# Kernel optimization log

Measured on AMD Instinct MI355X. Metric: run time of the kernel, lower is better.

Reference implementation:

```python
import jax, jax.numpy as jnp
import numpy as np

B, T, TR, D, H = 8, 1024, 256, 1024, 16
HS = D // H  # head size = 64
FF = 4 * D


def _ln(x, g, b, eps=1e-5):
    m = jnp.mean(x, axis=-1, keepdims=True)
    v = jnp.mean((x - m) ** 2, axis=-1, keepdims=True)
    return (x - m) * jax.lax.rsqrt(v + eps) * g + b


def setup_inputs() -> dict:
    key = jax.random.key(0)
    ks = jax.random.split(key, 24)
    w = lambda i, shape: jax.random.normal(ks[i], shape, dtype=jnp.float32) * 0.02
    return {
        "x": jax.random.normal(ks[0], (B, T, D), dtype=jnp.float32),
        # reduced positional embedding table (gathered by arange == table itself)
        "pos_emb": w(1, (TR, D)),
        # inner standard Block params
        "blk_ln1_g": jnp.ones((D,), jnp.float32), "blk_ln1_b": jnp.zeros((D,), jnp.float32),
        "blk_wq": w(2, (H, D, HS)), "blk_wk": w(3, (H, D, HS)), "blk_wv": w(4, (H, D, HS)),
        "blk_wo": w(5, (D, D)), "blk_bo": jnp.zeros((D,), jnp.float32),
        "blk_ln2_g": jnp.ones((D,), jnp.float32), "blk_ln2_b": jnp.zeros((D,), jnp.float32),
        "blk_w1": w(6, (D, FF)), "blk_b1": jnp.zeros((FF,), jnp.float32),
        "blk_w2": w(7, (FF, D)), "blk_b2": jnp.zeros((D,), jnp.float32),
        # compressing cross-attention params
        "ln1_g": jnp.ones((D,), jnp.float32), "ln1_b": jnp.zeros((D,), jnp.float32),
        "ca_wq": w(8, (H, D, HS)), "ca_wk": w(9, (H, D, HS)), "ca_wv": w(10, (H, D, HS)),
        "ca_wo": w(11, (D, D)), "ca_bo": jnp.zeros((D,), jnp.float32),
        "ln2_g": jnp.ones((D,), jnp.float32), "ln2_b": jnp.zeros((D,), jnp.float32),
        "ff_w1": w(12, (D, FF)), "ff_b1": jnp.zeros((FF,), jnp.float32),
        "ff_w2": w(13, (FF, D)), "ff_b2": jnp.zeros((D,), jnp.float32),
    }


def reference(x, pos_emb, blk_ln1_g, blk_ln1_b, blk_wq, blk_wk, blk_wv, blk_wo, blk_bo,
              blk_ln2_g, blk_ln2_b, blk_w1, blk_b1, blk_w2, blk_b2,
              ln1_g, ln1_b, ca_wq, ca_wk, ca_wv, ca_wo, ca_bo,
              ln2_g, ln2_b, ff_w1, ff_b1, ff_w2, ff_b2):
    b, t, c = x.shape
    scale = c ** -0.5  # matches q @ k^T * c**-0.5 in source

    # ---- inner standard Block: y = x + sa(ln1(x)); y = y + ffwd(ln2(y)) ----
    h = _ln(x, blk_ln1_g, blk_ln1_b)
    q = jnp.einsum('btc,hcs->bhts', h, blk_wq)
    k = jnp.einsum('btc,hcs->bhts', h, blk_wk)
    v = jnp.einsum('btc,hcs->bhts', h, blk_wv)
    wei = jnp.einsum('bhts,bhus->bhtu', q, k) * scale
    causal = jnp.tril(jnp.ones((t, t), dtype=bool))
    wei = jax.nn.softmax(jnp.where(causal, wei, -jnp.inf), axis=-1)
    att = jnp.einsum('bhtu,bhus->bhts', wei, v)
    att = att.transpose(0, 2, 1, 3).reshape(b, t, c) @ blk_wo + blk_bo
    y = x + att
    h2 = _ln(y, blk_ln2_g, blk_ln2_b)
    y = y + (jax.nn.relu(h2 @ blk_w1 + blk_b1) @ blk_w2 + blk_b2)

    # outer residual in CompressingBlock.forward
    x = x + y

    # ---- compressing cross-attention: queries/values from x, keys from pos emb ----
    h1 = _ln(x, ln1_g, ln1_b)
    q = jnp.einsum('btc,hcs->bhts', h1, ca_wq)
    kk = jnp.einsum('rc,hcs->hrs', pos_emb, ca_wk)  # same for every batch
    v = jnp.einsum('btc,hcs->bhts', h1, ca_wv)
    wei = jnp.einsum('bhts,hrs->bhtr', q, kk) * scale  # [b,h,t,tr]
    tr = pos_emb.shape[0]
    mask = jnp.tril(jnp.ones((t, tr), dtype=bool))  # tril[:t,:tr]
    wei = jax.nn.softmax(jnp.where(mask, wei, -jnp.inf), axis=-1)
    # transpose then wei^T @ v -> compressed sequence length tr
    out = jnp.einsum('bhtr,bhts->bhrs', wei, v)
    out = out.transpose(0, 2, 1, 3).reshape(b, tr, c) @ ca_wo + ca_bo

    # ---- final FFN with residual ----
    h3 = _ln(out, ln2_g, ln2_b)
    out = out + (jax.nn.relu(h3 @ ff_w1 + ff_b1) @ ff_w2 + ff_b2)
    return out
```

## Files before the change

### kernel.cpp

```cpp
#include <hip/hip_runtime.h>
#include <stdint.h>

typedef unsigned short u16;
typedef __attribute__((ext_vector_type(8))) short short8;
typedef __attribute__((ext_vector_type(4))) float f32x4;

#define MFMA16(A,B,C) __builtin_amdgcn_mfma_f32_16x16x32_bf16(A,B,C,0,0,0)

static __device__ __forceinline__ u16 f2bf(float f) {
  union { float f; unsigned u; } v; v.f = f;
  unsigned r = v.u + 0x7FFFu + ((v.u >> 16) & 1u);
  return (u16)(r >> 16);
}

static __device__ __forceinline__ void gload16(const void* g, void* l) {
  __builtin_amdgcn_global_load_lds(
      (const __attribute__((address_space(1))) void*)(uintptr_t)g,
      (__attribute__((address_space(3))) void*)(uint32_t)(uintptr_t)l,
      16, 0, 0);
}

static __device__ __forceinline__ int xcd_swz() {
  const int gx = gridDim.x, gy = gridDim.y, nwg = gx * gy;
  const int orig = blockIdx.y * gx + blockIdx.x;
  const int q = nwg >> 3, rm = nwg & 7, xcd = orig & 7, idx = orig >> 3;
  return (xcd < rm ? xcd * (q + 1) : rm * (q + 1) + (xcd - rm) * q) + idx;
}

#define PHASEP(BUFO, KH, STAGE_STMT, TAIL_STMT) do { \
  short8 af_[4], bf_[4]; \
  _Pragma("unroll") \
  for (int mf = 0; mf < 4; ++mf) { \
    const int r = wm0 + mf * 16 + colL; \
    af_[mf] = *(const short8*)&lds[(BUFO) + ((KH) << 12) + r * 32 + ((kgr ^ ((r >> 1) & 3)) << 3)]; \
  } \
  _Pragma("unroll") \
  for (int nf = 0; nf < 4; ++nf) { \
    const int r = wn0 + nf * 16 + colL; \
    bf_[nf] = *(const short8*)&lds[(BUFO) + 8192 + ((KH) << 12) + r * 32 + ((kgr ^ ((r >> 1) & 3)) << 3)]; \
  } \
  STAGE_STMT; \
  __builtin_amdgcn_s_barrier(); \
  asm volatile("s_waitcnt lgkmcnt(0)" ::: "memory"); \
  __builtin_amdgcn_sched_barrier(0); \
  __builtin_amdgcn_s_setprio(1); \
  _Pragma("unroll") \
  for (int mf = 0; mf < 4; ++mf) \
    _Pragma("unroll") \
    for (int nf = 0; nf < 4; ++nf) \
      acc[mf][nf] = MFMA16(af_[mf], bf_[nf], acc[mf][nf]); \
  __builtin_amdgcn_s_setprio(0); \
  __builtin_amdgcn_sched_barrier(0); \
  TAIL_STMT; \
  __builtin_amdgcn_s_barrier(); \
} while (0)

__global__ __launch_bounds__(256) void gemm128p(
    const u16* __restrict__ A, const u16* __restrict__ Wt,
    float* __restrict__ Cf, u16* __restrict__ Cb,
    const float* __restrict__ bias,
    const float* __restrict__ res1, const float* __restrict__ res2,
    int M, int N, int K, int relu)
{
  __shared__ u16 lds[32768];
  const int tid = threadIdx.x;
  const int wid = tid >> 6, lane = tid & 63;
  const int colL = lane & 15, kgr = lane >> 4;
  const int wm0 = (wid & 1) * 64, wn0 = (wid >> 1) * 64;
  const int w = xcd_swz();
  const int m0 = (w / gridDim.y) * 128, n0 = (w % gridDim.y) * 128;
  const int NT = K >> 6;
  f32x4 acc[4][4] = {};

  auto stageP = [&](int t_, int kh) {
    const int kb = t_ * 64 + kh * 32;
    const int baseA = ((t_ & 1) << 14) + (kh << 12);
#pragma unroll
    for (int i = 0; i < 2; ++i) {
      const int c = i * 256 + tid;
      const int row = c >> 2, slot = c & 3;
      const int cs = kb + ((slot ^ ((row >> 1) & 3)) << 3);
      gload16(A  + (size_t)(m0 + row) * K + cs,
              &lds[baseA + ((i * 256 + wid * 64) << 3)]);
      gload16(Wt + (size_t)(n0 + row) * K + cs,
              &lds[baseA + 8192 + ((i * 256 + wid * 64) << 3)]);
    }
  };

  stageP(0, 0); stageP(0, 1); stageP(1, 0);
  asm volatile("s_waitcnt vmcnt(8)" ::: "memory");
  __builtin_amdgcn_s_barrier();

  for (int t = 0; t < NT; ++t) {
    const int bufo = (t & 1) << 14;
    PHASEP(bufo, 0,
           if (t + 1 < NT) stageP(t + 1, 1),
           if (t + 1 < NT) { asm volatile("s_waitcnt vmcnt(8)" ::: "memory"); }
           else            { asm volatile("s_waitcnt vmcnt(0)" ::: "memory"); } );
    PHASEP(bufo, 1,
           if (t + 2 < NT) stageP(t + 2, 0),
           if (t < NT - 2)       { asm volatile("s_waitcnt vmcnt(8)" ::: "memory"); }
           else if (t == NT - 2) { asm volatile("s_waitcnt vmcnt(4)" ::: "memory"); }
           else                  { asm volatile("s_waitcnt vmcnt(0)" ::: "memory"); } );
  }

#pragma unroll
  for (int mf = 0; mf < 4; ++mf) {
#pragma unroll
    for (int nf = 0; nf < 4; ++nf) {
      const int n = n0 + wn0 + nf * 16 + colL;
      const float bv = bias ? bias[n] : 0.f;
#pragma unroll
      for (int rr = 0; rr < 4; ++rr) {
        const int m = m0 + wm0 + mf * 16 + kgr * 4 + rr;
        const size_t off = (size_t)m * N + n;
        float v = acc[mf][nf][rr] + bv;
        if (res1) v += res1[off];
        if (res2) v += res2[off];
        if (relu) v = fmaxf(v, 0.f);
        if (Cf) Cf[off] = v; else Cb[off] = f2bf(v);
      }
    }
  }
}

__global__ __launch_bounds__(256) void ln_rows(
    const float* __restrict__ x, const float* __restrict__ g,
    const float* __restrict__ bt, u16* __restrict__ out)
{
  const int row = blockIdx.x, tid = threadIdx.x;
  const float4 v = ((const float4*)(x + (size_t)row * 1024))[tid];
  float s  = v.x + v.y + v.z + v.w;
  float ss = v.x * v.x + v.y * v.y + v.z * v.z + v.w * v.w;
#pragma unroll
  for (int off = 32; off; off >>= 1) {
    s  += __shfl_xor(s, off);
    ss += __shfl_xor(ss, off);
  }
  __shared__ float red[8];
  const int wid = tid >> 6, lane = tid & 63;
  if (lane == 0) { red[wid] = s; red[4 + wid] = ss; }
  __syncthreads();
  s  = red[0] + red[1] + red[2] + red[3];
  ss = red[4] + red[5] + red[6] + red[7];
  const float mean = s * 0.0009765625f;
  const float var  = ss * 0.0009765625f - mean * mean;
  const float rstd = rsqrtf(var + 1e-5f);
  const float4 gg = ((const float4*)g)[tid];
  const float4 bb = ((const float4*)bt)[tid];
  uint2 ov;
  ov.x = (unsigned)f2bf((v.x - mean) * rstd * gg.x + bb.x) |
         ((unsigned)f2bf((v.y - mean) * rstd * gg.y + bb.y) << 16);
  ov.y = (unsigned)f2bf((v.z - mean) * rstd * gg.z + bb.z) |
         ((unsigned)f2bf((v.w - mean) * rstd * gg.w + bb.w) << 16);
  *(uint2*)(out + (size_t)row * 1024 + tid * 4) = ov;
}

__global__ __launch_bounds__(256) void transpose_w(
    const float* __restrict__ in, u16* __restrict__ out, int R, int C)
{
  __shared__ float t[32][33];
  const int c0 = blockIdx.x * 32, r0 = blockIdx.y * 32;
  const int tx = threadIdx.x & 31, ty = threadIdx.x >> 5;
#pragma unroll
  for (int i = 0; i < 32; i += 8)
    t[ty + i][tx] = in[(size_t)(r0 + ty + i) * C + c0 + tx];
  __syncthreads();
#pragma unroll
  for (int i = 0; i < 32; i += 8)
    out[(size_t)(c0 + ty + i) * R + r0 + tx] = f2bf(t[tx][ty + i]);
}

__global__ __launch_bounds__(256) void pack_head_w(
    const float* __restrict__ w, u16* __restrict__ out)
{
  __shared__ float t[32][33];
  const int h = blockIdx.z;
  const int s0 = blockIdx.x * 32, c0 = blockIdx.y * 32;
  const int tx = threadIdx.x & 31, ty = threadIdx.x >> 5;
#pragma unroll
  for (int i = 0; i < 32; i += 8)
    t[ty + i][tx] = w[((size_t)h * 1024 + c0 + ty + i) * 64 + s0 + tx];
  __syncthreads();
#pragma unroll
  for (int i = 0; i < 32; i += 8)
    out[((size_t)h * 64 + s0 + ty + i) * 1024 + c0 + tx] = f2bf(t[tx][ty + i]);
}

__global__ __launch_bounds__(256) void cvt_bf16(
    const float* __restrict__ in, u16* __restrict__ out)
{
  const int i = blockIdx.x * blockDim.x + threadIdx.x;
  const float4 v = ((const float4*)in)[i];
  uint2 ov;
  ov.x = (unsigned)f2bf(v.x) | ((unsigned)f2bf(v.y) << 16);
  ov.y = (unsigned)f2bf(v.z) | ((unsigned)f2bf(v.w) << 16);
  *(uint2*)(out + (size_t)i * 4) = ov;
}

__global__ __launch_bounds__(256) void vtrans(
    const u16* __restrict__ src, u16* __restrict__ dst, int coloff, int ld)
{
  __shared__ u16 tile[64][65];
  const int t0 = blockIdx.x * 64, h = blockIdx.y, b = blockIdx.z;
  const int lr = threadIdx.x >> 4;
  const int lc = (threadIdx.x & 15) * 4;
#pragma unroll
  for (int i = 0; i < 64; i += 16) {
    const u16* sp = src + (size_t)(b * 1024 + t0 + lr + i) * ld + coloff + h * 64 + lc;
    const uint2 v = *(const uint2*)sp;
    tile[lr + i][lc + 0] = (u16)(v.x & 0xffff);
    tile[lr + i][lc + 1] = (u16)(v.x >> 16);
    tile[lr + i][lc + 2] = (u16)(v.y & 0xffff);
    tile[lr + i][lc + 3] = (u16)(v.y >> 16);
  }
  __syncthreads();
#pragma unroll
  for (int i = 0; i < 64; i += 16) {
    const int s = lr + i;
    uint2 ov;
    ov.x = (unsigned)tile[lc + 0][s] | ((unsigned)tile[lc + 1][s] << 16);
    ov.y = (unsigned)tile[lc + 2][s] | ((unsigned)tile[lc + 3][s] << 16);
    *(uint2*)(dst + (size_t)((b * 16 + h) * 64 + s) * 1024 + t0 + lc) = ov;
  }
}

__global__ __launch_bounds__(512) void attn_inner(
    const u16* __restrict__ qkv, const u16* __restrict__ vt,
    u16* __restrict__ att)
{
  __shared__ u16 Kl[128 * 64];
  __shared__ u16 Vl[64 * 128];
  __shared__ u16 Pl[8 * 16 * 128];
  const int p = blockIdx.x, h = blockIdx.y, b = blockIdx.z;
  const int tid = threadIdx.x, wid = tid >> 6, lane = tid & 63;
  const int col = lane & 15, kgr = lane >> 4;
  const float scale = 0.03125f;
  u16* pw = &Pl[wid * 2048];

  auto run_q = [&](int tb) {
    short8 qf[2];
    {
      const int trow = tb * 128 + wid * 16 + col;
      const u16* qp = qkv + (size_t)(b * 1024 + trow) * 3072 + h * 64 + kgr * 8;
      qf[0] = *(const short8*)qp;
      qf[1] = *(const short8*)(qp + 32);
    }
    f32x4 o[4] = {};
    float mrun[4], lrun[4];
#pragma unroll
    for (int r = 0; r < 4; ++r) { mrun[r] = -1e30f; lrun[r] = 0.f; }

    for (int kt = 0; kt <= tb * 128; kt += 128) {
#pragma unroll
      for (int i = 0; i < 2; ++i) {
        const int e = i * 4096 + tid * 8;
        const int rk = e >> 6, uk = (e >> 3) & 7;
        gload16(qkv + (size_t)(b * 1024 + kt + rk) * 3072 + 1024 + h * 64 +
                    ((uk ^ (rk & 7)) << 3),
                &Kl[i * 4096 + wid * 512]);
        const int rv = e >> 7, uv = (e >> 3) & 15;
        gload16(vt + (size_t)((b * 16 + h) * 64 + rv) * 1024 + kt +
                    ((uv ^ (rv & 7)) << 3),
                &Vl[i * 4096 + wid * 512]);
      }
      __syncthreads();
      f32x4 s[8];
#pragma unroll
      for (int nt = 0; nt < 8; ++nt) {
        const int rk = nt * 16 + col;
        const short8 k0 = *(const short8*)&Kl[rk * 64 + ((kgr ^ (rk & 7)) << 3)];
        const short8 k1 = *(const short8*)&Kl[rk * 64 + (((kgr + 4) ^ (rk & 7)) << 3)];
        f32x4 a = {};
        a = MFMA16(qf[0], k0, a);
        a = MFMA16(qf[1], k1, a);
        s[nt] = a;
      }
      float mx[4];
#pragma unroll
      for (int r = 0; r < 4; ++r) mx[r] = -1e30f;
      const int tbase = tb * 128 + wid * 16 + kgr * 4;
      if (kt == tb * 128) {
#pragma unroll
        for (int nt = 0; nt < 8; ++nt) {
          const int kp = kt + nt * 16 + col;
#pragma unroll
          for (int r = 0; r < 4; ++r) {
            float v = s[nt][r] * scale;
            if (kp > tbase + r) v = -1e30f;
            s[nt][r] = v;
            mx[r] = fmaxf(mx[r], v);
          }
        }
      } else {
#pragma unroll
        for (int nt = 0; nt < 8; ++nt)
#pragma unroll
          for (int r = 0; r < 4; ++r) {
            const float v = s[nt][r] * scale;
            s[nt][r] = v;
            mx[r] = fmaxf(mx[r], v);
          }
      }
#pragma unroll
      for (int r = 0; r < 4; ++r)
#pragma unroll
        for (int off = 1; off < 16; off <<= 1)
          mx[r] = fmaxf(mx[r], __shfl_xor(mx[r], off));
      float f[4], rs[4];
#pragma unroll
      for (int r = 0; r < 4; ++r) {
        const float mn = fmaxf(mrun[r], mx[r]);
        f[r] = __expf(mrun[r] - mn);
        mrun[r] = mn;
        rs[r] = 0.f;
      }
#pragma unroll
      for (int nt = 0; nt < 8; ++nt)
#pragma unroll
        for (int r = 0; r < 4; ++r) {
          const float pv = __expf(s[nt][r] - mrun[r]);
          s[nt][r] = pv;
          rs[r] += pv;
        }
#pragma unroll
      for (int r = 0; r < 4; ++r) {
#pragma unroll
        for (int off = 1; off < 16; off <<= 1)
          rs[r] += __shfl_xor(rs[r], off);
        lrun[r] = lrun[r] * f[r] + rs[r];
      }
#pragma unroll
      for (int st = 0; st < 4; ++st)
#pragma unroll
        for (int r = 0; r < 4; ++r)
          o[st][r] *= f[r];
#pragma unroll
      for (int nt = 0; nt < 8; ++nt)
#pragma unroll
        for (int r = 0; r < 4; ++r) {
          const int rp = kgr * 4 + r;
          pw[rp * 128 + ((nt * 16 + col) ^ ((rp & 7) << 3))] = f2bf(s[nt][r]);
        }
#pragma unroll
      for (int ks = 0; ks < 4; ++ks) {
        const short8 pa = *(const short8*)&pw[col * 128 +
            ((ks * 32 + kgr * 8) ^ ((col & 7) << 3))];
#pragma unroll
        for (int st = 0; st < 4; ++st) {
          const int rv = st * 16 + col;
          const short8 vb = *(const short8*)&Vl[rv * 128 +
              (((ks * 4 + kgr) ^ (rv & 7)) << 3)];
          o[st] = MFMA16(pa, vb, o[st]);
        }
      }
      __syncthreads();
    }
#pragma unroll
    for (int r = 0; r < 4; ++r) {
      const float inv = 1.f / lrun[r];
      const int t = tb * 128 + wid * 16 + kgr * 4 + r;
#pragma unroll
      for (int st = 0; st < 4; ++st)
        att[(size_t)(b * 1024 + t) * 1024 + h * 64 + st * 16 + col] =
            f2bf(o[st][r] * inv);
    }
  };

  run_q(7 - p);
  run_q(p);
}

__global__ __launch_bounds__(512) void attn_cross(
    const u16* __restrict__ qv, const u16* __restrict__ kk,
    const u16* __restrict__ vt, u16* __restrict__ outc)
{
  __shared__ u16 KKl[256 * 64];
  __shared__ u16 Vl[64 * 128];
  __shared__ u16 PTl[256 * 128];
  const int h = blockIdx.x, b = blockIdx.y;
  const int tid = threadIdx.x, wid = tid >> 6, lane = tid & 63;
  const int col = lane & 15, kgr = lane >> 4;
  const float scale = 0.03125f;
#pragma unroll
  for (int i = 0; i < 4; ++i) {
    const int e = i * 4096 + tid * 8;
    const int rk = e >> 6, uk = (e >> 3) & 7;
    gload16(kk + (size_t)rk * 1024 + h * 64 + ((uk ^ (rk & 7)) << 3),
            &KKl[i * 4096 + wid * 512]);
  }
  f32x4 oacc[2][4] = {};
  for (int tt = 0; tt < 8; ++tt) {
    const int t0 = tt * 128;
#pragma unroll
    for (int i = 0; i < 2; ++i) {
      const int e = i * 4096 + tid * 8;
      const int rv = e >> 7, uv = (e >> 3) & 15;
      gload16(vt + (size_t)((b * 16 + h) * 64 + rv) * 1024 + t0 +
                  ((uv ^ (rv & 7)) << 3),
              &Vl[i * 4096 + wid * 512]);
    }
    short8 qf0, qf1;
    {
      const int trow = t0 + wid * 16 + col;
      const u16* qp = qv + (size_t)(b * 1024 + trow) * 2048 + h * 64 + kgr * 8;
      qf0 = *(const short8*)qp;
      qf1 = *(const short8*)(qp + 32);
    }
    __syncthreads();
    f32x4 s[16];
#pragma unroll
    for (int rt = 0; rt < 16; ++rt) {
      const int rk = rt * 16 + col;
      const short8 k0 = *(const short8*)&KKl[rk * 64 + ((kgr ^ (rk & 7)) << 3)];
      const short8 k1 = *(const short8*)&KKl[rk * 64 + (((kgr + 4) ^ (rk & 7)) << 3)];
      f32x4 a = {};
      a = MFMA16(qf0, k0, a);
      a = MFMA16(qf1, k1, a);
      s[rt] = a;
    }
    float mx[4];
#pragma unroll
    for (int r = 0; r < 4; ++r) mx[r] = -1e30f;
    const int tbase = t0 + wid * 16 + kgr * 4;
    if (t0 < 256) {
#pragma unroll
      for (int rt = 0; rt < 16; ++rt) {
        const int rp = rt * 16 + col;
#pragma unroll
        for (int r = 0; r < 4; ++r) {
          float v = s[rt][r] * scale;
          if (rp > tbase + r) v = -1e30f;
          s[rt][r] = v;
          mx[r] = fmaxf(mx[r], v);
        }
      }
    } else {
#pragma unroll
      for (int rt = 0; rt < 16; ++rt)
#pragma unroll
        for (int r = 0; r < 4; ++r) {
          const float v = s[rt][r] * scale;
          s[rt][r] = v;
          mx[r] = fmaxf(mx[r], v);
        }
    }
#pragma unroll
    for (int r = 0; r < 4; ++r)
#pragma unroll
      for (int off = 1; off < 16; off <<= 1)
        mx[r] = fmaxf(mx[r], __shfl_xor(mx[r], off));
    float sm[4];
#pragma unroll
    for (int r = 0; r < 4; ++r) sm[r] = 0.f;
#pragma unroll
    for (int rt = 0; rt < 16; ++rt)
#pragma unroll
      for (int r = 0; r < 4; ++r) {
        const float pv = __expf(s[rt][r] - mx[r]);
        s[rt][r] = pv;
        sm[r] += pv;
      }
#pragma unroll
    for (int r = 0; r < 4; ++r) {
#pragma unroll
      for (int off = 1; off < 16; off <<= 1)
        sm[r] += __shfl_xor(sm[r], off);
      sm[r] = 1.f / sm[r];
    }
#pragma unroll
    for (int rt = 0; rt < 16; ++rt)
#pragma unroll
      for (int r = 0; r < 4; ++r) {
        const int rpt = rt * 16 + col;
        PTl[rpt * 128 + ((wid * 16 + kgr * 4 + r) ^ ((rpt & 7) << 3))] =
            f2bf(s[rt][r] * sm[r]);
      }
    __syncthreads();
#pragma unroll
    for (int rr = 0; rr < 2; ++rr) {
      const int rb = (wid * 2 + rr) * 16;
#pragma unroll
      for (int ks = 0; ks < 4; ++ks) {
        const int rpt = rb + col;
        const short8 pa = *(const short8*)&PTl[rpt * 128 +
            ((ks * 32 + kgr * 8) ^ ((rpt & 7) << 3))];
#pragma unroll
        for (int st = 0; st < 4; ++st) {
          const int rv = st * 16 + col;
          const short8 vb = *(const short8*)&Vl[rv * 128 +
              (((ks * 4 + kgr) ^ (rv & 7)) << 3)];
          oacc[rr][st] = MFMA16(pa, vb, oacc[rr][st]);
        }
      }
    }
    __syncthreads();
  }
#pragma unroll
  for (int rr = 0; rr < 2; ++rr)
#pragma unroll
    for (int st = 0; st < 4; ++st)
#pragma unroll
      for (int r = 0; r < 4; ++r) {
        const int rpos = (wid * 2 + rr) * 16 + kgr * 4 + r;
        outc[(size_t)(b * 256 + rpos) * 1024 + h * 64 + st * 16 + col] =
            f2bf(oacc[rr][st][r]);
      }
}

extern "C" void kernel_launch(void* const* d_in, const int* in_sizes, int n_in,
                              void* d_out, int out_size, void* d_ws, size_t ws_size,
                              hipStream_t stream)
{
  const float* x     = (const float*)d_in[0];
  const float* pos   = (const float*)d_in[1];
  const float* bln1g = (const float*)d_in[2];
  const float* bln1b = (const float*)d_in[3];
  const float* bwq   = (const float*)d_in[4];
  const float* bwk   = (const float*)d_in[5];
  const float* bwv   = (const float*)d_in[6];
  const float* bwo   = (const float*)d_in[7];
  const float* bbo   = (const float*)d_in[8];
  const float* bln2g = (const float*)d_in[9];
  const float* bln2b = (const float*)d_in[10];
  const float* bw1   = (const float*)d_in[11];
  const float* bb1   = (const float*)d_in[12];
  const float* bw2   = (const float*)d_in[13];
  const float* bb2   = (const float*)d_in[14];
  const float* ln1g  = (const float*)d_in[15];
  const float* ln1b  = (const float*)d_in[16];
  const float* cwq   = (const float*)d_in[17];
  const float* cwk   = (const float*)d_in[18];
  const float* cwv   = (const float*)d_in[19];
  const float* cwo   = (const float*)d_in[20];
  const float* cbo   = (const float*)d_in[21];
  const float* cln2g = (const float*)d_in[22];
  const float* cln2b = (const float*)d_in[23];
  const float* fw1   = (const float*)d_in[24];
  const float* fb1   = (const float*)d_in[25];
  const float* fw2   = (const float*)d_in[26];
  const float* fb2   = (const float*)d_in[27];

  char* ws = (char*)d_ws;
  size_t off = 0;
  auto alloc = [&](size_t bytes) -> void* {
    void* p = ws + off; off += (bytes + 255) & ~(size_t)255; return p;
  };
  u16* wqkv_t = (u16*)alloc((size_t)3072 * 1024 * 2);
  u16* wo_t   = (u16*)alloc((size_t)1024 * 1024 * 2);
  u16* w1_t   = (u16*)alloc((size_t)4096 * 1024 * 2);
  u16* w2_t   = (u16*)alloc((size_t)1024 * 4096 * 2);
  u16* cwqv_t = (u16*)alloc((size_t)2048 * 1024 * 2);
  u16* cwk_t  = (u16*)alloc((size_t)1024 * 1024 * 2);
  u16* cwo_t  = (u16*)alloc((size_t)1024 * 1024 * 2);
  u16* fw1_t  = (u16*)alloc((size_t)4096 * 1024 * 2);
  u16* fw2_t  = (u16*)alloc((size_t)1024 * 4096 * 2);
  u16* pos_bf = (u16*)alloc((size_t)256 * 1024 * 2);
  u16* kkb    = (u16*)alloc((size_t)256 * 1024 * 2);
  u16* act_ln = (u16*)alloc((size_t)8192 * 1024 * 2);
  u16* qkv    = (u16*)alloc((size_t)8192 * 3072 * 2);
  u16* att    = (u16*)alloc((size_t)8192 * 1024 * 2);
  u16* ffb    = (u16*)alloc((size_t)8192 * 4096 * 2);
  float* yb   = (float*)alloc((size_t)8192 * 1024 * 4);
  if (ws_size < off) return;
  float* x2   = (float*)qkv;
  u16*   qv   = qkv;
  u16*   vt   = ffb;
  u16*   outc = att;
  float* zb   = yb;
  float* outp = (float*)d_out;

  const dim3 B256(256), B512(512);
  pack_head_w<<<dim3(2, 32, 16), B256, 0, stream>>>(bwq, wqkv_t);
  pack_head_w<<<dim3(2, 32, 16), B256, 0, stream>>>(bwk, wqkv_t + 1024 * 1024);
  pack_head_w<<<dim3(2, 32, 16), B256, 0, stream>>>(bwv, wqkv_t + 2048 * 1024);
  transpose_w<<<dim3(32, 32),  B256, 0, stream>>>(bwo, wo_t, 1024, 1024);
  transpose_w<<<dim3(128, 32), B256, 0, stream>>>(bw1, w1_t, 1024, 4096);
  transpose_w<<<dim3(32, 128), B256, 0, stream>>>(bw2, w2_t, 4096, 1024);
  pack_head_w<<<dim3(2, 32, 16), B256, 0, stream>>>(cwq, cwqv_t);
  pack_head_w<<<dim3(2, 32, 16), B256, 0, stream>>>(cwv, cwqv_t + 1024 * 1024);
  pack_head_w<<<dim3(2, 32, 16), B256, 0, stream>>>(cwk, cwk_t);
  transpose_w<<<dim3(32, 32),  B256, 0, stream>>>(cwo, cwo_t, 1024, 1024);
  transpose_w<<<dim3(128, 32), B256, 0, stream>>>(fw1, fw1_t, 1024, 4096);
  transpose_w<<<dim3(32, 128), B256, 0, stream>>>(fw2, fw2_t, 4096, 1024);
  cvt_bf16<<<dim3(256), B256, 0, stream>>>(pos, pos_bf);

  ln_rows<<<dim3(8192), B256, 0, stream>>>(x, bln1g, bln1b, act_ln);
  gemm128p<<<dim3(64, 24), B256, 0, stream>>>(act_ln, wqkv_t, nullptr, qkv,
      nullptr, nullptr, nullptr, 8192, 3072, 1024, 0);
  vtrans<<<dim3(16, 16, 8), B256, 0, stream>>>(qkv, vt, 2048, 3072);
  attn_inner<<<dim3(4, 16, 8), B512, 0, stream>>>(qkv, vt, att);
  gemm128p<<<dim3(64, 8), B256, 0, stream>>>(att, wo_t, yb, nullptr,
      bbo, x, nullptr, 8192, 1024, 1024, 0);
  ln_rows<<<dim3(8192), B256, 0, stream>>>(yb, bln2g, bln2b, act_ln);
  gemm128p<<<dim3(64, 32), B256, 0, stream>>>(act_ln, w1_t, nullptr, ffb,
      bb1, nullptr, nullptr, 8192, 4096, 1024, 1);
  gemm128p<<<dim3(64, 8), B256, 0, stream>>>(ffb, w2_t, x2, nullptr,
      bb2, yb, x, 8192, 1024, 4096, 0);

  ln_rows<<<dim3(8192), B256, 0, stream>>>(x2, ln1g, ln1b, act_ln);
  gemm128p<<<dim3(64, 16), B256, 0, stream>>>(act_ln, cwqv_t, nullptr, qv,
      nullptr, nullptr, nullptr, 8192, 2048, 1024, 0);
  gemm128p<<<dim3(2, 8), B256, 0, stream>>>(pos_bf, cwk_t, nullptr, kkb,
      nullptr, nullptr, nullptr, 256, 1024, 1024, 0);
  vtrans<<<dim3(16, 16, 8), B256, 0, stream>>>(qv, vt, 1024, 2048);
  attn_cross<<<dim3(16, 8), B512, 0, stream>>>(qv, kkb, vt, outc);
  gemm128p<<<dim3(16, 8), B256, 0, stream>>>(outc, cwo_t, zb, nullptr,
      cbo, nullptr, nullptr, 2048, 1024, 1024, 0);

  ln_rows<<<dim3(2048), B256, 0, stream>>>(zb, cln2g, cln2b, act_ln);
  gemm128p<<<dim3(16, 32), B256, 0, stream>>>(act_ln, fw1_t, nullptr, ffb,
      fb1, nullptr, nullptr, 2048, 4096, 1024, 1);
  gemm128p<<<dim3(16, 8), B256, 0, stream>>>(ffb, fw2_t, outp, nullptr,
      fb2, zb, nullptr, 2048, 1024, 4096, 0);
}
```

Measured before the change: 720.3 us.

## Load GEMM A operand directly from global into registers, stage only B in LDS

The bf16 GEMM kernel stops staging the A tile through LDS. Each wave now reads its A fragments directly from global memory into registers, double-buffered across the K half-steps, while only the weight (B) tile still goes through LDS via global_load_lds. This halves LDS use and raises the launch-bounds occupancy hint to 3 blocks per CU, aiming to cut LDS traffic and overlap more work. In exchange, A reads from global are less coalesced and are duplicated across waves that share rows, and their latency sits directly in front of the MFMAs. The vmcnt wait counts were retuned to match the new load mix.

```diff
diff --git a/kernel.cpp b/kernel.cpp
--- a/kernel.cpp
+++ b/kernel.cpp
@@ -27,19 +27,14 @@
   return (xcd < rm ? xcd * (q + 1) : rm * (q + 1) + (xcd - rm) * q) + idx;
 }
 
-#define PHASEP(BUFO, KH, STAGE_STMT, TAIL_STMT) do { \
-  short8 af_[4], bf_[4]; \
-  _Pragma("unroll") \
-  for (int mf = 0; mf < 4; ++mf) { \
-    const int r = wm0 + mf * 16 + colL; \
-    af_[mf] = *(const short8*)&lds[(BUFO) + ((KH) << 12) + r * 32 + ((kgr ^ ((r >> 1) & 3)) << 3)]; \
-  } \
+#define GPHASE(BUFO, KH, AF, PRE_STMT, TAIL_STMT) do { \
+  short8 bf_[4]; \
   _Pragma("unroll") \
   for (int nf = 0; nf < 4; ++nf) { \
     const int r = wn0 + nf * 16 + colL; \
-    bf_[nf] = *(const short8*)&lds[(BUFO) + 8192 + ((KH) << 12) + r * 32 + ((kgr ^ ((r >> 1) & 3)) << 3)]; \
+    bf_[nf] = *(const short8*)&lds[(BUFO) + ((KH) << 12) + r * 32 + ((kgr ^ ((r >> 1) & 3)) << 3)]; \
   } \
-  STAGE_STMT; \
+  PRE_STMT; \
   __builtin_amdgcn_s_barrier(); \
   asm volatile("s_waitcnt lgkmcnt(0)" ::: "memory"); \
   __builtin_amdgcn_sched_barrier(0); \
@@ -48,21 +43,21 @@
   for (int mf = 0; mf < 4; ++mf) \
     _Pragma("unroll") \
     for (int nf = 0; nf < 4; ++nf) \
-      acc[mf][nf] = MFMA16(af_[mf], bf_[nf], acc[mf][nf]); \
+      acc[mf][nf] = MFMA16(AF[mf], bf_[nf], acc[mf][nf]); \
   __builtin_amdgcn_s_setprio(0); \
   __builtin_amdgcn_sched_barrier(0); \
   TAIL_STMT; \
   __builtin_amdgcn_s_barrier(); \
 } while (0)
 
-__global__ __launch_bounds__(256) void gemm128p(
+__global__ __launch_bounds__(256, 3) void gemm128p(
     const u16* __restrict__ A, const u16* __restrict__ Wt,
     float* __restrict__ Cf, u16* __restrict__ Cb,
     const float* __restrict__ bias,
     const float* __restrict__ res1, const float* __restrict__ res2,
     int M, int N, int K, int relu)
 {
-  __shared__ u16 lds[32768];
+  __shared__ u16 lds[16384];
   const int tid = threadIdx.x;
   const int wid = tid >> 6, lane = tid & 63;
   const int colL = lane & 15, kgr = lane >> 4;
@@ -72,36 +67,49 @@
   const int NT = K >> 6;
   f32x4 acc[4][4] = {};
 
-  auto stageP = [&](int t_, int kh) {
+  const u16* ap0 = A + (size_t)(m0 + wm0 +  0 + colL) * K + kgr * 8;
+  const u16* ap1 = A + (size_t)(m0 + wm0 + 16 + colL) * K + kgr * 8;
+  const u16* ap2 = A + (size_t)(m0 + wm0 + 32 + colL) * K + kgr * 8;
+  const u16* ap3 = A + (size_t)(m0 + wm0 + 48 + colL) * K + kgr * 8;
+
+  auto stageB = [&](int t_, int kh) {
     const int kb = t_ * 64 + kh * 32;
-    const int baseA = ((t_ & 1) << 14) + (kh << 12);
+    const int base = ((t_ & 1) << 13) + (kh << 12);
 #pragma unroll
     for (int i = 0; i < 2; ++i) {
       const int c = i * 256 + tid;
       const int row = c >> 2, slot = c & 3;
-      const int cs = kb + ((slot ^ ((row >> 1) & 3)) << 3);
-      gload16(A  + (size_t)(m0 + row) * K + cs,
-              &lds[baseA + ((i * 256 + wid * 64) << 3)]);
-      gload16(Wt + (size_t)(n0 + row) * K + cs,
-              &lds[baseA + 8192 + ((i * 256 + wid * 64) << 3)]);
+      gload16(Wt + (size_t)(n0 + row) * K + kb + ((slot ^ ((row >> 1) & 3)) << 3),
+              &lds[base + ((i * 256 + wid * 64) << 3)]);
     }
   };
 
-  stageP(0, 0); stageP(0, 1); stageP(1, 0);
-  asm volatile("s_waitcnt vmcnt(8)" ::: "memory");
+  short8 afA[4], afB[4];
+  auto loadA = [&](short8* dst, int t_, int kh) {
+    const int ko = t_ * 64 + kh * 32;
+    dst[0] = *(const short8*)(ap0 + ko);
+    dst[1] = *(const short8*)(ap1 + ko);
+    dst[2] = *(const short8*)(ap2 + ko);
+    dst[3] = *(const short8*)(ap3 + ko);
+  };
+
+  stageB(0, 0); stageB(0, 1); stageB(1, 0);
+  asm volatile("s_waitcnt vmcnt(4)" ::: "memory");
+  loadA(afA, 0, 0);
   __builtin_amdgcn_s_barrier();
 
   for (int t = 0; t < NT; ++t) {
-    const int bufo = (t & 1) << 14;
-    PHASEP(bufo, 0,
-           if (t + 1 < NT) stageP(t + 1, 1),
-           if (t + 1 < NT) { asm volatile("s_waitcnt vmcnt(8)" ::: "memory"); }
-           else            { asm volatile("s_waitcnt vmcnt(0)" ::: "memory"); } );
-    PHASEP(bufo, 1,
-           if (t + 2 < NT) stageP(t + 2, 0),
-           if (t < NT - 2)       { asm volatile("s_waitcnt vmcnt(8)" ::: "memory"); }
-           else if (t == NT - 2) { asm volatile("s_waitcnt vmcnt(4)" ::: "memory"); }
-           else                  { asm volatile("s_waitcnt vmcnt(0)" ::: "memory"); } );
+    const int bufo = (t & 1) << 13;
+    GPHASE(bufo, 0, afA,
+           { if (t + 1 < NT) stageB(t + 1, 1); loadA(afB, t, 1); },
+           { if (t + 1 < NT) { asm volatile("s_waitcnt vmcnt(12)" ::: "memory"); }
+             else            { asm volatile("s_waitcnt vmcnt(8)"  ::: "memory"); } });
+    GPHASE(bufo, 1, afB,
+           { if (t + 2 < NT) stageB(t + 2, 0);
+             if (t + 1 < NT) loadA(afA, t + 1, 0); },
+           { if (t + 2 < NT)      { asm volatile("s_waitcnt vmcnt(12)" ::: "memory"); }
+             else if (t + 1 < NT) { asm volatile("s_waitcnt vmcnt(10)" ::: "memory"); }
+             else                 { asm volatile("s_waitcnt vmcnt(0)"  ::: "memory"); } });
   }
 
 #pragma unroll
```

Result: slower. 1.028 ms (+42.7%).

## Switch GEMMs to 256x128 tiles with triple-buffered K=32 LDS pipeline

Applied to the files above, without the earlier changes.

Replaces the 128x128 double-buffered GEMM with a 256x128 tile where each wave computes 128x64 (8x4 MFMA fragments). The K loop now stages 32-wide slices into three rotating LDS buffers with a two-deep prefetch. Launch bounds ask for two blocks per CU. The larger M tile raises arithmetic intensity and halves the number of blocks. In exchange it doubles accumulator registers and produces fewer workgroups for the small 2048-row and 256-row GEMMs.

```diff
diff --git a/kernel.cpp b/kernel.cpp
--- a/kernel.cpp
+++ b/kernel.cpp
@@ -27,17 +27,17 @@
   return (xcd < rm ? xcd * (q + 1) : rm * (q + 1) + (xcd - rm) * q) + idx;
 }
 
-#define PHASEP(BUFO, KH, STAGE_STMT, TAIL_STMT) do { \
-  short8 af_[4], bf_[4]; \
+#define GPH(CUR, STAGE_STMT, TAIL_STMT) do { \
+  short8 af_[8], bf_[4]; \
   _Pragma("unroll") \
-  for (int mf = 0; mf < 4; ++mf) { \
+  for (int mf = 0; mf < 8; ++mf) { \
     const int r = wm0 + mf * 16 + colL; \
-    af_[mf] = *(const short8*)&lds[(BUFO) + ((KH) << 12) + r * 32 + ((kgr ^ ((r >> 1) & 3)) << 3)]; \
+    af_[mf] = *(const short8*)&lds[(CUR) + r * 32 + ((kgr ^ ((r >> 1) & 3)) << 3)]; \
   } \
   _Pragma("unroll") \
   for (int nf = 0; nf < 4; ++nf) { \
     const int r = wn0 + nf * 16 + colL; \
-    bf_[nf] = *(const short8*)&lds[(BUFO) + 8192 + ((KH) << 12) + r * 32 + ((kgr ^ ((r >> 1) & 3)) << 3)]; \
+    bf_[nf] = *(const short8*)&lds[(CUR) + (256 + r) * 32 + ((kgr ^ ((r >> 1) & 3)) << 3)]; \
   } \
   STAGE_STMT; \
   __builtin_amdgcn_s_barrier(); \
@@ -45,7 +45,7 @@
   __builtin_amdgcn_sched_barrier(0); \
   __builtin_amdgcn_s_setprio(1); \
   _Pragma("unroll") \
-  for (int mf = 0; mf < 4; ++mf) \
+  for (int mf = 0; mf < 8; ++mf) \
     _Pragma("unroll") \
     for (int nf = 0; nf < 4; ++nf) \
       acc[mf][nf] = MFMA16(af_[mf], bf_[nf], acc[mf][nf]); \
@@ -55,57 +55,56 @@
   __builtin_amdgcn_s_barrier(); \
 } while (0)
 
-__global__ __launch_bounds__(256) void gemm128p(
+__global__ __launch_bounds__(256, 2) void gemm256n(
     const u16* __restrict__ A, const u16* __restrict__ Wt,
     float* __restrict__ Cf, u16* __restrict__ Cb,
     const float* __restrict__ bias,
     const float* __restrict__ res1, const float* __restrict__ res2,
     int M, int N, int K, int relu)
 {
-  __shared__ u16 lds[32768];
+  __shared__ u16 lds[36864];
   const int tid = threadIdx.x;
   const int wid = tid >> 6, lane = tid & 63;
   const int colL = lane & 15, kgr = lane >> 4;
-  const int wm0 = (wid & 1) * 64, wn0 = (wid >> 1) * 64;
+  const int wm0 = (wid & 1) * 128, wn0 = (wid >> 1) * 64;
   const int w = xcd_swz();
-  const int m0 = (w / gridDim.y) * 128, n0 = (w % gridDim.y) * 128;
-  const int NT = K >> 6;
-  f32x4 acc[4][4] = {};
-
-  auto stageP = [&](int t_, int kh) {
-    const int kb = t_ * 64 + kh * 32;
-    const int baseA = ((t_ & 1) << 14) + (kh << 12);
-#pragma unroll
-    for (int i = 0; i < 2; ++i) {
+  const int m0 = (w / gridDim.y) * 256, n0 = (w % gridDim.y) * 128;
+  const int NT = K >> 5;
+  f32x4 acc[8][4] = {};
+
+  auto stage = [&](int t_, int bufo) {
+    const int kb = t_ * 32;
+#pragma unroll
+    for (int i = 0; i < 4; ++i) {
       const int c = i * 256 + tid;
       const int row = c >> 2, slot = c & 3;
-      const int cs = kb + ((slot ^ ((row >> 1) & 3)) << 3);
-      gload16(A  + (size_t)(m0 + row) * K + cs,
-              &lds[baseA + ((i * 256 + wid * 64) << 3)]);
-      gload16(Wt + (size_t)(n0 + row) * K + cs,
-              &lds[baseA + 8192 + ((i * 256 + wid * 64) << 3)]);
+      gload16(A + (size_t)(m0 + row) * K + kb + ((slot ^ ((row >> 1) & 3)) << 3),
+              &lds[bufo + ((i * 256 + wid * 64) << 3)]);
+    }
+#pragma unroll
+    for (int i = 4; i < 6; ++i) {
+      const int c = i * 256 + tid;
+      const int row = c >> 2, slot = c & 3;
+      gload16(Wt + (size_t)(n0 + row - 256) * K + kb + ((slot ^ ((row >> 1) & 3)) << 3),
+              &lds[bufo + ((i * 256 + wid * 64) << 3)]);
     }
   };
 
-  stageP(0, 0); stageP(0, 1); stageP(1, 0);
-  asm volatile("s_waitcnt vmcnt(8)" ::: "memory");
+  int c0 = 0, c1 = 12288, c2 = 24576;
+  stage(0, c0); stage(1, c1);
+  asm volatile("s_waitcnt vmcnt(6)" ::: "memory");
   __builtin_amdgcn_s_barrier();
 
   for (int t = 0; t < NT; ++t) {
-    const int bufo = (t & 1) << 14;
-    PHASEP(bufo, 0,
-           if (t + 1 < NT) stageP(t + 1, 1),
-           if (t + 1 < NT) { asm volatile("s_waitcnt vmcnt(8)" ::: "memory"); }
-           else            { asm volatile("s_waitcnt vmcnt(0)" ::: "memory"); } );
-    PHASEP(bufo, 1,
-           if (t + 2 < NT) stageP(t + 2, 0),
-           if (t < NT - 2)       { asm volatile("s_waitcnt vmcnt(8)" ::: "memory"); }
-           else if (t == NT - 2) { asm volatile("s_waitcnt vmcnt(4)" ::: "memory"); }
-           else                  { asm volatile("s_waitcnt vmcnt(0)" ::: "memory"); } );
+    GPH(c0,
+        { if (t + 2 < NT) stage(t + 2, c2); },
+        { if (t + 2 < NT) { asm volatile("s_waitcnt vmcnt(6)" ::: "memory"); }
+          else            { asm volatile("s_waitcnt vmcnt(0)" ::: "memory"); } });
+    const int tmp = c0; c0 = c1; c1 = c2; c2 = tmp;
   }
 
 #pragma unroll
-  for (int mf = 0; mf < 4; ++mf) {
+  for (int mf = 0; mf < 8; ++mf) {
 #pragma unroll
     for (int nf = 0; nf < 4; ++nf) {
       const int n = n0 + wn0 + nf * 16 + colL;
@@ -586,31 +585,31 @@
   cvt_bf16<<<dim3(256), B256, 0, stream>>>(pos, pos_bf);
 
   ln_rows<<<dim3(8192), B256, 0, stream>>>(x, bln1g, bln1b, act_ln);
-  gemm128p<<<dim3(64, 24), B256, 0, stream>>>(act_ln, wqkv_t, nullptr, qkv,
+  gemm256n<<<dim3(32, 24), B256, 0, stream>>>(act_ln, wqkv_t, nullptr, qkv,
       nullptr, nullptr, nullptr, 8192, 3072, 1024, 0);
   vtrans<<<dim3(16, 16, 8), B256, 0, stream>>>(qkv, vt, 2048, 3072);
   attn_inner<<<dim3(4, 16, 8), B512, 0, stream>>>(qkv, vt, att);
-  gemm128p<<<dim3(64, 8), B256, 0, stream>>>(att, wo_t, yb, nullptr,
+  gemm256n<<<dim3(32, 8), B256, 0, stream>>>(att, wo_t, yb, nullptr,
       bbo, x, nullptr, 8192, 1024, 1024, 0);
   ln_rows<<<dim3(8192), B256, 0, stream>>>(yb, bln2g, bln2b, act_ln);
-  gemm128p<<<dim3(64, 32), B256, 0, stream>>>(act_ln, w1_t, nullptr, ffb,
+  gemm256n<<<dim3(32, 32), B256, 0, stream>>>(act_ln, w1_t, nullptr, ffb,
       bb1, nullptr, nullptr, 8192, 4096, 1024, 1);
-  gemm128p<<<dim3(64, 8), B256, 0, stream>>>(ffb, w2_t, x2, nullptr,
+  gemm256n<<<dim3(32, 8), B256, 0, stream>>>(ffb, w2_t, x2, nullptr,
       bb2, yb, x, 8192, 1024, 4096, 0);
 
   ln_rows<<<dim3(8192), B256, 0, stream>>>(x2, ln1g, ln1b, act_ln);
-  gemm128p<<<dim3(64, 16), B256, 0, stream>>>(act_ln, cwqv_t, nullptr, qv,
+  gemm256n<<<dim3(32, 16), B256, 0, stream>>>(act_ln, cwqv_t, nullptr, qv,
       nullptr, nullptr, nullptr, 8192, 2048, 1024, 0);
-  gemm128p<<<dim3(2, 8), B256, 0, stream>>>(pos_bf, cwk_t, nullptr, kkb,
+  gemm256n<<<dim3(1, 8), B256, 0, stream>>>(pos_bf, cwk_t, nullptr, kkb,
       nullptr, nullptr, nullptr, 256, 1024, 1024, 0);
   vtrans<<<dim3(16, 16, 8), B256, 0, stream>>>(qv, vt, 1024, 2048);
   attn_cross<<<dim3(16, 8), B512, 0, stream>>>(qv, kkb, vt, outc);
-  gemm128p<<<dim3(16, 8), B256, 0, stream>>>(outc, cwo_t, zb, nullptr,
+  gemm256n<<<dim3(8, 8), B256, 0, stream>>>(outc, cwo_t, zb, nullptr,
       cbo, nullptr, nullptr, 2048, 1024, 1024, 0);
 
   ln_rows<<<dim3(2048), B256, 0, stream>>>(zb, cln2g, cln2b, act_ln);
-  gemm128p<<<dim3(16, 32), B256, 0, stream>>>(act_ln, fw1_t, nullptr, ffb,
+  gemm256n<<<dim3(8, 32), B256, 0, stream>>>(act_ln, fw1_t, nullptr, ffb,
       fb1, nullptr, nullptr, 2048, 4096, 1024, 1);
-  gemm128p<<<dim3(16, 8), B256, 0, stream>>>(ffb, fw2_t, outp, nullptr,
+  gemm256n<<<dim3(8, 8), B256, 0, stream>>>(ffb, fw2_t, outp, nullptr,
       fb2, zb, nullptr, 2048, 1024, 4096, 0);
 }
```

After: 800.6 us. 11.2% more time.

## Restructure GEMM K-loop into triple-buffered rotating LDS stages of 32

Applied to the files above, without the earlier changes.

Replaces the double-buffered 64-wide K tile (split into two 32-wide halves) with a three-slot ring of 32-wide K stages that rotate each iteration, prefetching two stages ahead. LDS use drops from 64KB to 48KB per block, which may allow higher occupancy and simplifies the wait-count logic. In exchange the in-flight prefetch depth is slightly lower (one stage of loads outstanding vs. two halves) and the loop runs twice as many iterations.

```diff
diff --git a/kernel.cpp b/kernel.cpp
--- a/kernel.cpp
+++ b/kernel.cpp
@@ -27,17 +27,17 @@
   return (xcd < rm ? xcd * (q + 1) : rm * (q + 1) + (xcd - rm) * q) + idx;
 }
 
-#define PHASEP(BUFO, KH, STAGE_STMT, TAIL_STMT) do { \
+#define GPH(CUR, STAGE_STMT, TAIL_STMT) do { \
   short8 af_[4], bf_[4]; \
   _Pragma("unroll") \
   for (int mf = 0; mf < 4; ++mf) { \
     const int r = wm0 + mf * 16 + colL; \
-    af_[mf] = *(const short8*)&lds[(BUFO) + ((KH) << 12) + r * 32 + ((kgr ^ ((r >> 1) & 3)) << 3)]; \
+    af_[mf] = *(const short8*)&lds[(CUR) + r * 32 + ((kgr ^ ((r >> 1) & 3)) << 3)]; \
   } \
   _Pragma("unroll") \
   for (int nf = 0; nf < 4; ++nf) { \
     const int r = wn0 + nf * 16 + colL; \
-    bf_[nf] = *(const short8*)&lds[(BUFO) + 8192 + ((KH) << 12) + r * 32 + ((kgr ^ ((r >> 1) & 3)) << 3)]; \
+    bf_[nf] = *(const short8*)&lds[(CUR) + 4096 + r * 32 + ((kgr ^ ((r >> 1) & 3)) << 3)]; \
   } \
   STAGE_STMT; \
   __builtin_amdgcn_s_barrier(); \
@@ -62,46 +62,41 @@
     const float* __restrict__ res1, const float* __restrict__ res2,
     int M, int N, int K, int relu)
 {
-  __shared__ u16 lds[32768];
+  __shared__ u16 lds[24576];
   const int tid = threadIdx.x;
   const int wid = tid >> 6, lane = tid & 63;
   const int colL = lane & 15, kgr = lane >> 4;
   const int wm0 = (wid & 1) * 64, wn0 = (wid >> 1) * 64;
   const int w = xcd_swz();
   const int m0 = (w / gridDim.y) * 128, n0 = (w % gridDim.y) * 128;
-  const int NT = K >> 6;
+  const int U = K >> 5;
   f32x4 acc[4][4] = {};
 
-  auto stageP = [&](int t_, int kh) {
-    const int kb = t_ * 64 + kh * 32;
-    const int baseA = ((t_ & 1) << 14) + (kh << 12);
+  auto stageP = [&](int u, int bufo) {
+    const int kb = u * 32;
 #pragma unroll
     for (int i = 0; i < 2; ++i) {
       const int c = i * 256 + tid;
       const int row = c >> 2, slot = c & 3;
       const int cs = kb + ((slot ^ ((row >> 1) & 3)) << 3);
       gload16(A  + (size_t)(m0 + row) * K + cs,
-              &lds[baseA + ((i * 256 + wid * 64) << 3)]);
+              &lds[bufo + ((i * 256 + wid * 64) << 3)]);
       gload16(Wt + (size_t)(n0 + row) * K + cs,
-              &lds[baseA + 8192 + ((i * 256 + wid * 64) << 3)]);
+              &lds[bufo + 4096 + ((i * 256 + wid * 64) << 3)]);
     }
   };
 
-  stageP(0, 0); stageP(0, 1); stageP(1, 0);
-  asm volatile("s_waitcnt vmcnt(8)" ::: "memory");
+  int c0 = 0, c1 = 8192, c2 = 16384;
+  stageP(0, c0); stageP(1, c1);
+  asm volatile("s_waitcnt vmcnt(4)" ::: "memory");
   __builtin_amdgcn_s_barrier();
 
-  for (int t = 0; t < NT; ++t) {
-    const int bufo = (t & 1) << 14;
-    PHASEP(bufo, 0,
-           if (t + 1 < NT) stageP(t + 1, 1),
-           if (t + 1 < NT) { asm volatile("s_waitcnt vmcnt(8)" ::: "memory"); }
-           else            { asm volatile("s_waitcnt vmcnt(0)" ::: "memory"); } );
-    PHASEP(bufo, 1,
-           if (t + 2 < NT) stageP(t + 2, 0),
-           if (t < NT - 2)       { asm volatile("s_waitcnt vmcnt(8)" ::: "memory"); }
-           else if (t == NT - 2) { asm volatile("s_waitcnt vmcnt(4)" ::: "memory"); }
-           else                  { asm volatile("s_waitcnt vmcnt(0)" ::: "memory"); } );
+  for (int u = 0; u < U; ++u) {
+    GPH(c0,
+        { if (u + 2 < U) stageP(u + 2, c2); },
+        { if (u + 2 < U) { asm volatile("s_waitcnt vmcnt(4)" ::: "memory"); }
+          else           { asm volatile("s_waitcnt vmcnt(0)" ::: "memory"); } });
+    const int tmp = c0; c0 = c1; c1 = c2; c2 = tmp;
   }
 
 #pragma unroll
```

After: 699.5 us. -2.9%, faster.
